# Kernel tuning notes

Hardware: AMD Instinct MI355X
Metric: run time of the kernel (lower is better)

## Reference

```python
import jax, jax.numpy as jnp
import numpy as np

T, B, I, H, R = 24, 64, 128, 256, 64
CLIP_VAL = 1.0
LN_EPS = 1e-5


def _ln(x, g, b):
    mu = jnp.mean(x, axis=-1, keepdims=True)
    var = jnp.mean(jnp.square(x - mu), axis=-1, keepdims=True)
    return (x - mu) / jnp.sqrt(var + LN_EPS) * g + b


def setup_inputs() -> dict:
    key = jax.random.key(0)
    ks = jax.random.split(key, 12)
    x = jax.random.normal(ks[0], (T, B, I), dtype=jnp.float32)
    h0 = 0.1 * jax.random.normal(ks[1], (B, H), dtype=jnp.float32)
    v0 = 0.1 * jax.random.normal(ks[2], (B, H), dtype=jnp.float32)
    dU0 = 0.01 * jax.random.normal(ks[3], (B, H, H), dtype=jnp.float32)
    trace_e0 = 0.1 * jax.random.normal(ks[4], (B, H), dtype=jnp.float32)
    trace_E0 = 0.01 * jax.random.normal(ks[5], (B, H, H), dtype=jnp.float32)
    # parameters, initialized like the torch module
    x2h_w = jax.random.normal(ks[6], (H + R, I), dtype=jnp.float32) / np.sqrt(I)
    x2h_b = jnp.zeros((H + R,), dtype=jnp.float32)
    h2h_w = jax.random.normal(ks[7], (H + R, H), dtype=jnp.float32) / np.sqrt(H)
    h2h_b = jnp.zeros((H + R,), dtype=jnp.float32)
    lnx_g = jnp.ones((H + R,), dtype=jnp.float32)
    lnx_b = jnp.zeros((H + R,), dtype=jnp.float32)
    lnh_g = jnp.ones((H + R,), dtype=jnp.float32)
    lnh_b = jnp.zeros((H + R,), dtype=jnp.float32)
    alpha = 0.01 * jnp.ones((1, H, H), dtype=jnp.float32)
    mod2h = jnp.ones((1, H, R), dtype=jnp.float32) / R
    tau_v = -jnp.log(1.0 + 5.0 * jax.random.uniform(ks[8], (1, H), dtype=jnp.float32))
    tau_U = -2.0 * jnp.ones((1, H, H), dtype=jnp.float32)
    tau_E = -1.0 * jnp.ones((1, H, H), dtype=jnp.float32)
    return dict(x=x, h0=h0, v0=v0, dU0=dU0, trace_e0=trace_e0, trace_E0=trace_E0,
                x2h_w=x2h_w, x2h_b=x2h_b, h2h_w=h2h_w, h2h_b=h2h_b,
                lnx_g=lnx_g, lnx_b=lnx_b, lnh_g=lnh_g, lnh_b=lnh_b,
                alpha=alpha, mod2h=mod2h, tau_v=tau_v, tau_U=tau_U, tau_E=tau_E)


def reference(x, h0, v0, dU0, trace_e0, trace_E0,
              x2h_w, x2h_b, h2h_w, h2h_b,
              lnx_g, lnx_b, lnh_g, lnh_b,
              alpha, mod2h, tau_v, tau_U, tau_E):
    ra = jax.nn.relu(alpha)                      # [1,H,H]
    sv = jax.nn.sigmoid(tau_v)                   # [1,H]
    sU = jax.nn.sigmoid(tau_U)                   # [1,H,H]
    sE = jax.nn.sigmoid(tau_E)                   # [1,H,H]
    W_hh = h2h_w[:H, :]                          # [H,H]
    denom = ra + 1e-8
    dU_hi = jax.nn.relu(CLIP_VAL - W_hh) / denom  # [1,H,H]
    dU_lo = -jax.nn.relu(CLIP_VAL + W_hh) / denom

    def step(carry, x_t):
        v, h, dU, te, tE = carry
        Wx = _ln(x_t @ x2h_w.T + x2h_b, lnx_g, lnx_b)   # [B,H+R]
        Wh = _ln(h @ h2h_w.T + h2h_b, lnh_g, lnh_b)     # [B,H+R]
        dv = Wx[:, :H] + Wh[:, :H] + jnp.einsum('bij,bj->bi', ra * dU, h)
        v = (1.0 - sv) * v + sv * dv
        nh = jax.nn.relu(v)                              # activation='relu'
        mod = jnp.einsum('hr,br->bh', mod2h[0], jax.nn.relu(Wx[:, H:] + Wh[:, H:]))
        nte = (1.0 - sv) * te + sv * h
        ntE = (1.0 - sE) * tE + sE * (nh[:, :, None] * te[:, None, :]
                                      - nte[:, :, None] * h[:, None, :])
        dU = (1.0 - sU) * dU + sU * mod[:, :, None] * ntE
        dU = jnp.maximum(jnp.minimum(dU, dU_hi), dU_lo)
        return (v, nh, dU, nte, ntE), nh

    (v, h, dU, te, tE), out = jax.lax.scan(step, (v0, h0, dU0, trace_e0, trace_E0), x)
    return (v, h, dU, te, tE, out)
```

## Files before the change

### kernel.cpp

```cpp
#include <hip/hip_runtime.h>

#define T_STEPS 24
#define BB 64
#define I_DIM 128
#define HH 256
#define RR 64
#define HR 320

__global__ __launch_bounds__(256) void k_init_const(
    const float* __restrict__ alpha, const float* __restrict__ tau_U,
    const float* __restrict__ tau_E, const float* __restrict__ tau_v,
    const float* __restrict__ h2h_w,
    float* __restrict__ ra, float* __restrict__ sU, float* __restrict__ sE,
    float* __restrict__ hi, float* __restrict__ lo, float* __restrict__ sv)
{
    int idx = blockIdx.x * 256 + threadIdx.x;
    if (idx >= HH * HH) return;
    float a = alpha[idx]; a = a > 0.f ? a : 0.f;
    ra[idx] = a;
    sU[idx] = 1.f / (1.f + expf(-tau_U[idx]));
    sE[idx] = 1.f / (1.f + expf(-tau_E[idx]));
    float wv = h2h_w[idx];
    float inv = 1.f / (a + 1e-8f);
    float hi_ = 1.0f - wv; hi_ = hi_ > 0.f ? hi_ : 0.f;
    float lo_ = 1.0f + wv; lo_ = lo_ > 0.f ? lo_ : 0.f;
    hi[idx] = hi_ * inv;
    lo[idx] = -lo_ * inv;
    if (idx < HH) sv[idx] = 1.f / (1.f + expf(-tau_v[idx]));
}

__global__ __launch_bounds__(HR) void k_wx(
    const float* __restrict__ x,
    const float* __restrict__ w,
    const float* __restrict__ bias,
    const float* __restrict__ g, const float* __restrict__ be,
    float* __restrict__ Wx)
{
    __shared__ float xs[I_DIM];
    __shared__ float rs[5], rs2[5];
    int row = blockIdx.x;
    int p = threadIdx.x;
    if (p < I_DIM) xs[p] = x[(size_t)row * I_DIM + p];
    __syncthreads();
    const float* wr = w + (size_t)p * I_DIM;
    float acc = bias[p];
    #pragma unroll 8
    for (int k = 0; k < I_DIM; k += 4)
        acc += wr[k]*xs[k] + wr[k+1]*xs[k+1] + wr[k+2]*xs[k+2] + wr[k+3]*xs[k+3];
    float s = acc, s2 = acc * acc;
    int lane = p & 63, wv = p >> 6;
    for (int off = 32; off > 0; off >>= 1) { s += __shfl_down(s, off); s2 += __shfl_down(s2, off); }
    if (lane == 0) { rs[wv] = s; rs2[wv] = s2; }
    __syncthreads();
    float sum = 0.f, sum2 = 0.f;
    #pragma unroll
    for (int q = 0; q < 5; q++) { sum += rs[q]; sum2 += rs2[q]; }
    float mu = sum * (1.f / HR);
    float rstd = rsqrtf(sum2 * (1.f / HR) - mu * mu + 1e-5f);
    Wx[(size_t)row * HR + p] = (acc - mu) * rstd * g[p] + be[p];
}

__global__ __launch_bounds__(256) void k_s0(
    const float* __restrict__ dU0, const float* __restrict__ h0,
    const float* __restrict__ ra, float* __restrict__ s_out)
{
    int r = blockIdx.x * 4 + (threadIdx.x >> 6);
    int lane = threadIdx.x & 63;
    int b = r >> 8, i = r & 255;
    float4 du = ((const float4*)dU0)[(size_t)r * 64 + lane];
    float4 rv = ((const float4*)ra)[(size_t)i * 64 + lane];
    float4 hv = ((const float4*)h0)[(size_t)b * 64 + lane];
    float acc = rv.x*du.x*hv.x + rv.y*du.y*hv.y + rv.z*du.z*hv.z + rv.w*du.w*hv.w;
    for (int off = 32; off > 0; off >>= 1) acc += __shfl_down(acc, off);
    if (lane == 0) s_out[r] = acc;
}

__global__ __launch_bounds__(HR) void k_step_a(
    const float* __restrict__ h_old,
    const float* __restrict__ v_old,
    const float* __restrict__ te_old,
    const float* __restrict__ Wx_t,
    const float* __restrict__ s_in,
    const float* __restrict__ h2h_w,
    const float* __restrict__ h2h_b,
    const float* __restrict__ lnh_g, const float* __restrict__ lnh_b,
    const float* __restrict__ sv,
    const float* __restrict__ mod2h,
    float* __restrict__ v_out,
    float* __restrict__ nh_out,
    float* __restrict__ nte_out,
    float* __restrict__ mod_out)
{
    __shared__ float hs[HH];
    __shared__ float modin[RR];
    __shared__ float rs[5], rs2[5];
    int b = blockIdx.x;
    int p = threadIdx.x;
    if (p < HH) hs[p] = h_old[(size_t)b * HH + p];
    __syncthreads();
    const float* wr = h2h_w + (size_t)p * HH;
    float acc = h2h_b[p];
    #pragma unroll 8
    for (int k = 0; k < HH; k += 4)
        acc += wr[k]*hs[k] + wr[k+1]*hs[k+1] + wr[k+2]*hs[k+2] + wr[k+3]*hs[k+3];
    float s = acc, s2 = acc * acc;
    int lane = p & 63, wv = p >> 6;
    for (int off = 32; off > 0; off >>= 1) { s += __shfl_down(s, off); s2 += __shfl_down(s2, off); }
    if (lane == 0) { rs[wv] = s; rs2[wv] = s2; }
    __syncthreads();
    float sum = 0.f, sum2 = 0.f;
    #pragma unroll
    for (int q = 0; q < 5; q++) { sum += rs[q]; sum2 += rs2[q]; }
    float mu = sum * (1.f / HR);
    float rstd = rsqrtf(sum2 * (1.f / HR) - mu * mu + 1e-5f);
    float wh = (acc - mu) * rstd * lnh_g[p] + lnh_b[p];
    float wx = Wx_t[(size_t)b * HR + p];
    if (p >= HH) {
        float m = wx + wh;
        modin[p - HH] = m > 0.f ? m : 0.f;
    } else {
        float dv = wx + wh + s_in[(size_t)b * HH + p];
        float svp = sv[p];
        float v = (1.f - svp) * v_old[(size_t)b * HH + p] + svp * dv;
        v_out[(size_t)b * HH + p] = v;
        float nh = v > 0.f ? v : 0.f;
        nh_out[(size_t)b * HH + p] = nh;
        nte_out[(size_t)b * HH + p] = (1.f - svp) * te_old[(size_t)b * HH + p] + svp * hs[p];
    }
    __syncthreads();
    if (p < HH) {
        const float* m2 = mod2h + (size_t)p * RR;
        float mm = 0.f;
        #pragma unroll 8
        for (int r = 0; r < RR; r += 4)
            mm += m2[r]*modin[r] + m2[r+1]*modin[r+1] + m2[r+2]*modin[r+2] + m2[r+3]*modin[r+3];
        mod_out[(size_t)b * HH + p] = mm;
    }
}

__global__ __launch_bounds__(256) void k_step_b(
    const float* __restrict__ dU_old, float* __restrict__ dU_new,
    const float* __restrict__ tE_old, float* __restrict__ tE_new,
    const float* __restrict__ nh,
    const float* __restrict__ h_old,
    const float* __restrict__ te_old,
    const float* __restrict__ nte,
    const float* __restrict__ mod,
    const float* __restrict__ ra, const float* __restrict__ sU,
    const float* __restrict__ sE, const float* __restrict__ hi,
    const float* __restrict__ lo,
    float* __restrict__ s_out)
{
    int r = blockIdx.x * 4 + (threadIdx.x >> 6);
    int lane = threadIdx.x & 63;
    int b = r >> 8, i = r & 255;
    size_t rowv = (size_t)r * 64 + lane;
    size_t cv   = (size_t)i * 64 + lane;
    size_t bv   = (size_t)b * 64 + lane;
    float4 du  = ((const float4*)dU_old)[rowv];
    float4 tE  = ((const float4*)tE_old)[rowv];
    float4 raV = ((const float4*)ra)[cv];
    float4 sUV = ((const float4*)sU)[cv];
    float4 sEV = ((const float4*)sE)[cv];
    float4 hiV = ((const float4*)hi)[cv];
    float4 loV = ((const float4*)lo)[cv];
    float4 teV = ((const float4*)te_old)[bv];
    float4 hV  = ((const float4*)h_old)[bv];
    float4 nhJ = ((const float4*)nh)[bv];
    float nhi  = nh[(size_t)b * HH + i];
    float ntei = nte[(size_t)b * HH + i];
    float modi = mod[(size_t)b * HH + i];

    float4 ntE, ndu;
    float acc = 0.f;
#define COMPONENT(c)                                                        \
    {                                                                       \
        float e = (1.f - sEV.c) * tE.c + sEV.c * (nhi * teV.c - ntei * hV.c); \
        float d = (1.f - sUV.c) * du.c + sUV.c * modi * e;                  \
        d = fminf(d, hiV.c); d = fmaxf(d, loV.c);                           \
        ntE.c = e; ndu.c = d;                                               \
        acc += raV.c * d * nhJ.c;                                           \
    }
    COMPONENT(x) COMPONENT(y) COMPONENT(z) COMPONENT(w)
#undef COMPONENT
    ((float4*)tE_new)[rowv] = ntE;
    ((float4*)dU_new)[rowv] = ndu;
    for (int off = 32; off > 0; off >>= 1) acc += __shfl_down(acc, off);
    if (lane == 0) s_out[r] = acc;
}

extern "C" void kernel_launch(void* const* d_in, const int* in_sizes, int n_in,
                              void* d_out, int out_size, void* d_ws, size_t ws_size,
                              hipStream_t stream)
{
    const float* x     = (const float*)d_in[0];
    const float* h0    = (const float*)d_in[1];
    const float* v0    = (const float*)d_in[2];
    const float* dU0   = (const float*)d_in[3];
    const float* te0   = (const float*)d_in[4];
    const float* tE0   = (const float*)d_in[5];
    const float* x2h_w = (const float*)d_in[6];
    const float* x2h_b = (const float*)d_in[7];
    const float* h2h_w = (const float*)d_in[8];
    const float* h2h_b = (const float*)d_in[9];
    const float* lnx_g = (const float*)d_in[10];
    const float* lnx_b = (const float*)d_in[11];
    const float* lnh_g = (const float*)d_in[12];
    const float* lnh_b = (const float*)d_in[13];
    const float* alpha = (const float*)d_in[14];
    const float* mod2h = (const float*)d_in[15];
    const float* tau_v = (const float*)d_in[16];
    const float* tau_U = (const float*)d_in[17];
    const float* tau_E = (const float*)d_in[18];

    float* out  = (float*)d_out;
    float* o_v  = out;
    float* o_h  = out + 16384;
    float* o_dU = out + 32768;
    float* o_te = out + 4227072;
    float* o_tE = out + 4243456;
    float* o_out= out + 8437760;

    float* w = (float*)d_ws;
    float* Wx  = w;  w += (size_t)T_STEPS * BB * HR;
    float* ra  = w;  w += HH * HH;
    float* sU  = w;  w += HH * HH;
    float* sE  = w;  w += HH * HH;
    float* hi  = w;  w += HH * HH;
    float* lo  = w;  w += HH * HH;
    float* sv  = w;  w += 256;
    float* s_buf = w; w += BB * HH;
    float* modb  = w; w += BB * HH;
    float* nteb0 = w; w += BB * HH;
    float* nteb1 = w; w += BB * HH;
    float* nteb[2] = { nteb0, nteb1 };

    k_init_const<<<256, 256, 0, stream>>>(alpha, tau_U, tau_E, tau_v, h2h_w,
                                          ra, sU, sE, hi, lo, sv);
    k_wx<<<T_STEPS * BB, HR, 0, stream>>>(x, x2h_w, x2h_b, lnx_g, lnx_b, Wx);
    k_s0<<<4096, 256, 0, stream>>>(dU0, h0, ra, s_buf);

    for (int t = 0; t < T_STEPS; t++) {
        const float* h_old  = (t == 0) ? h0  : o_out + (size_t)(t - 1) * BB * HH;
        const float* v_old  = (t == 0) ? v0  : o_v;
        const float* te_oldp= (t == 0) ? te0 : nteb[(t + 1) & 1];
        const float* dUo    = (t == 0) ? dU0 : o_dU;
        const float* tEo    = (t == 0) ? tE0 : o_tE;
        float* nh = o_out + (size_t)t * BB * HH;
        k_step_a<<<BB, HR, 0, stream>>>(h_old, v_old, te_oldp,
                                        Wx + (size_t)t * BB * HR, s_buf,
                                        h2h_w, h2h_b, lnh_g, lnh_b, sv, mod2h,
                                        o_v, nh, nteb[t & 1], modb);
        k_step_b<<<4096, 256, 0, stream>>>(dUo, o_dU, tEo, o_tE, nh, h_old,
                                           te_oldp, nteb[t & 1], modb,
                                           ra, sU, sE, hi, lo, s_buf);
    }
    hipMemcpyAsync(o_h,  o_out + (size_t)(T_STEPS - 1) * BB * HH, (size_t)BB * HH * 4,
                   hipMemcpyDeviceToDevice, stream);
    hipMemcpyAsync(o_te, nteb[(T_STEPS - 1) & 1], (size_t)BB * HH * 4,
                   hipMemcpyDeviceToDevice, stream);
}
```

Before: 799.3 us.

## Fuse recurrent scan into one persistent cooperative kernel with register-resident state

Replaces the 48 per-timestep kernel launches with a single cooperative persistent kernel of 512 blocks (8 per batch row). Each block keeps its slice of dU and trace_E in registers for all 24 steps, so the two large B×H×H tensors are read once and written once instead of every step. The h2h matvec for the next step is split across blocks, and steps are separated by grid-wide syncs. This adds grid.sync latency per step and heavy register pressure, and keeps the old multi-launch path as a fallback if the cooperative launch fails.

```diff
diff --git a/kernel.cpp b/kernel.cpp
--- a/kernel.cpp
+++ b/kernel.cpp
@@ -1,4 +1,7 @@
 #include <hip/hip_runtime.h>
+#include <hip/hip_cooperative_groups.h>
+
+namespace cg = cooperative_groups;
 
 #define T_STEPS 24
 #define BB 64
@@ -30,8 +33,7 @@
 }
 
 __global__ __launch_bounds__(HR) void k_wx(
-    const float* __restrict__ x,
-    const float* __restrict__ w,
+    const float* __restrict__ x, const float* __restrict__ w,
     const float* __restrict__ bias,
     const float* __restrict__ g, const float* __restrict__ be,
     float* __restrict__ Wx)
@@ -75,21 +77,208 @@
     if (lane == 0) s_out[r] = acc;
 }
 
+__global__ __launch_bounds__(HR) void k_wh0(
+    const float* __restrict__ h0, const float* __restrict__ w,
+    const float* __restrict__ bias, float* __restrict__ whp)
+{
+    __shared__ float hs[HH];
+    int b = blockIdx.x, p = threadIdx.x;
+    if (p < HH) hs[p] = h0[(size_t)b * HH + p];
+    __syncthreads();
+    const float* wr = w + (size_t)p * HH;
+    float acc = bias[p];
+    #pragma unroll 8
+    for (int k = 0; k < HH; k += 4)
+        acc += wr[k]*hs[k] + wr[k+1]*hs[k+1] + wr[k+2]*hs[k+2] + wr[k+3]*hs[k+3];
+    whp[(size_t)b * HR + p] = acc;
+}
+
+__global__ __launch_bounds__(256, 2) void k_scan(
+    const float* __restrict__ dU0, const float* __restrict__ tE0,
+    const float* __restrict__ h0, const float* __restrict__ v0,
+    const float* __restrict__ te0,
+    const float* __restrict__ Wx,
+    const float* __restrict__ h2h_w, const float* __restrict__ h2h_b,
+    const float* __restrict__ lnh_g, const float* __restrict__ lnh_b,
+    const float* __restrict__ sv_g,
+    const float* __restrict__ mod2h,
+    const float* __restrict__ ra, const float* __restrict__ sU,
+    const float* __restrict__ sE, const float* __restrict__ hi,
+    const float* __restrict__ lo,
+    float* __restrict__ whpA, float* __restrict__ whpB,
+    float* __restrict__ sbufA, float* __restrict__ sbufB,
+    float* __restrict__ o_v, float* __restrict__ o_h, float* __restrict__ o_dU,
+    float* __restrict__ o_te, float* __restrict__ o_tE, float* __restrict__ o_out)
+{
+    cg::grid_group grid = cg::this_grid();
+
+    __shared__ __align__(16) float sh_h[2][HH];
+    __shared__ __align__(16) float sh_te[2][HH];
+    __shared__ float sh_v[HH];
+    __shared__ __align__(16) float sh_modin[RR];
+    __shared__ float sh_red[4], sh_red2[4];
+
+    const int bk  = blockIdx.x;
+    const int b   = bk >> 3;
+    const int g   = bk & 7;
+    const int tid = threadIdx.x;
+    const int row_local = tid >> 4;
+    const int jg  = tid & 15;
+    const int i0  = g * 32 + row_local;
+    const int wv  = tid >> 6;
+    const int lane = tid & 63;
+
+    const float svp = sv_g[tid];
+    const float g0 = lnh_g[tid],  be0 = lnh_b[tid];
+    float g1 = 0.f, be1 = 0.f;
+    if (tid < 64) { g1 = lnh_g[HH + tid]; be1 = lnh_b[HH + tid]; }
+
+    const size_t rbase = ((size_t)(b * HH + i0)) * 64 + jg;
+    const float4* dU0v = (const float4*)dU0;
+    const float4* tE0v = (const float4*)tE0;
+    float4 du[2][4], tEr[2][4];
+    #pragma unroll
+    for (int r = 0; r < 2; ++r) {
+        const size_t rb = rbase + (size_t)r * (16 * 64);
+        #pragma unroll
+        for (int k = 0; k < 4; ++k) {
+            du[r][k]  = dU0v[rb + k * 16];
+            tEr[r][k] = tE0v[rb + k * 16];
+        }
+    }
+
+    const float4* raV4 = (const float4*)ra;
+    const float4* sUV4 = (const float4*)sU;
+    const float4* sEV4 = (const float4*)sE;
+    const float4* hiV4 = (const float4*)hi;
+    const float4* loV4 = (const float4*)lo;
+
+    sh_h[0][tid]  = h0[(size_t)b * HH + tid];
+    sh_te[0][tid] = te0[(size_t)b * HH + tid];
+    sh_v[tid]     = v0[(size_t)b * HH + tid];
+    __syncthreads();
+
+    #pragma unroll 1
+    for (int t = 0; t < T_STEPS; t++) {
+        const int cur = t & 1, nxt = cur ^ 1;
+        const float* whp  = (cur == 0) ? whpA  : whpB;
+        float*       whpn = (cur == 0) ? whpB  : whpA;
+        const float* sbi  = (cur == 0) ? sbufA : sbufB;
+        float*       sbo  = (cur == 0) ? sbufB : sbufA;
+
+        const float* whb = whp + (size_t)b * HR;
+        float p0 = whb[tid];
+        float p1 = (tid < 64) ? whb[HH + tid] : 0.f;
+        float s = p0 + p1, s2 = p0 * p0 + p1 * p1;
+        #pragma unroll
+        for (int off = 32; off > 0; off >>= 1) { s += __shfl_down(s, off); s2 += __shfl_down(s2, off); }
+        if (lane == 0) { sh_red[wv] = s; sh_red2[wv] = s2; }
+        __syncthreads();
+        float sum = sh_red[0] + sh_red[1] + sh_red[2] + sh_red[3];
+        float sum2 = sh_red2[0] + sh_red2[1] + sh_red2[2] + sh_red2[3];
+        float mu = sum * (1.f / HR);
+        float rstd = rsqrtf(sum2 * (1.f / HR) - mu * mu + 1e-5f);
+
+        const float* wx_t = Wx + ((size_t)t * BB + b) * HR;
+        float wh0 = (p0 - mu) * rstd * g0 + be0;
+        float dv = wx_t[tid] + wh0 + sbi[(size_t)b * HH + tid];
+        float vnew = (1.f - svp) * sh_v[tid] + svp * dv;
+        sh_v[tid] = vnew;
+        float nh = vnew > 0.f ? vnew : 0.f;
+        sh_h[nxt][tid] = nh;
+        sh_te[nxt][tid] = (1.f - svp) * sh_te[cur][tid] + svp * sh_h[cur][tid];
+        if (tid < 64) {
+            float wh1 = (p1 - mu) * rstd * g1 + be1;
+            float m = wx_t[HH + tid] + wh1;
+            sh_modin[tid] = m > 0.f ? m : 0.f;
+        }
+        if (g == 0) o_out[((size_t)t * BB + b) * HH + tid] = nh;
+        __syncthreads();
+
+#define COMPONENT(c, jj) { \
+        float teO = sh_te[cur][jj]; float hO = sh_h[cur][jj]; float nhJ = sh_h[nxt][jj]; \
+        float e = (1.f - sEV.c) * TE.c + sEV.c * (nhi * teO - ntei * hO); \
+        float d = (1.f - sUV.c) * DU.c + sUV.c * modi * e; \
+        d = fminf(d, hiV.c); d = fmaxf(d, loV.c); \
+        TE.c = e; DU.c = d; acc += raV.c * d * nhJ; }
+
+        #pragma unroll
+        for (int r = 0; r < 2; ++r) {
+            const int i = i0 + r * 16;
+            float4 m4 = *(const float4*)(mod2h + (size_t)i * RR + jg * 4);
+            float4 mi = *(const float4*)&sh_modin[jg * 4];
+            float macc = m4.x*mi.x + m4.y*mi.y + m4.z*mi.z + m4.w*mi.w;
+            macc += __shfl_down(macc, 8, 16);
+            macc += __shfl_down(macc, 4, 16);
+            macc += __shfl_down(macc, 2, 16);
+            macc += __shfl_down(macc, 1, 16);
+            const float modi = __shfl(macc, 0, 16);
+            const float nhi  = sh_h[nxt][i];
+            const float ntei = sh_te[nxt][i];
+            float acc = 0.f;
+            #pragma unroll
+            for (int k = 0; k < 4; ++k) {
+                const size_t ci = (size_t)i * 64 + jg + k * 16;
+                const float4 raV = raV4[ci]; const float4 sUV = sUV4[ci];
+                const float4 sEV = sEV4[ci]; const float4 hiV = hiV4[ci];
+                const float4 loV = loV4[ci];
+                float4 &DU = du[r][k];
+                float4 &TE = tEr[r][k];
+                const int j0 = k * 64 + jg * 4;
+                COMPONENT(x, j0 + 0) COMPONENT(y, j0 + 1)
+                COMPONENT(z, j0 + 2) COMPONENT(w, j0 + 3)
+            }
+            acc += __shfl_down(acc, 8, 16);
+            acc += __shfl_down(acc, 4, 16);
+            acc += __shfl_down(acc, 2, 16);
+            acc += __shfl_down(acc, 1, 16);
+            if (jg == 0) sbo[(size_t)b * HH + i] = acc;
+        }
+#undef COMPONENT
+
+        if (t != T_STEPS - 1) {
+            #pragma unroll
+            for (int k = 0; k < 10; k++) {
+                int p = g * 40 + wv + 4 * k;
+                float4 wrow = ((const float4*)(h2h_w + (size_t)p * HH))[lane];
+                float4 hv = *(const float4*)&sh_h[nxt][lane * 4];
+                float d = wrow.x*hv.x + wrow.y*hv.y + wrow.z*hv.z + wrow.w*hv.w;
+                #pragma unroll
+                for (int off = 32; off > 0; off >>= 1) d += __shfl_down(d, off);
+                if (lane == 0) whpn[(size_t)b * HR + p] = d + h2h_b[p];
+            }
+            __threadfence();
+            grid.sync();
+        }
+    }
+
+    if (g == 0) {
+        o_v[(size_t)b * HH + tid]  = sh_v[tid];
+        o_h[(size_t)b * HH + tid]  = sh_h[0][tid];
+        o_te[(size_t)b * HH + tid] = sh_te[0][tid];
+    }
+    float4* o_dUv = (float4*)o_dU;
+    float4* o_tEv = (float4*)o_tE;
+    #pragma unroll
+    for (int r = 0; r < 2; ++r) {
+        const size_t rb = rbase + (size_t)r * (16 * 64);
+        #pragma unroll
+        for (int k = 0; k < 4; ++k) {
+            o_dUv[rb + k * 16] = du[r][k];
+            o_tEv[rb + k * 16] = tEr[r][k];
+        }
+    }
+}
+
 __global__ __launch_bounds__(HR) void k_step_a(
-    const float* __restrict__ h_old,
-    const float* __restrict__ v_old,
-    const float* __restrict__ te_old,
-    const float* __restrict__ Wx_t,
+    const float* __restrict__ h_old, const float* __restrict__ v_old,
+    const float* __restrict__ te_old, const float* __restrict__ Wx_t,
     const float* __restrict__ s_in,
-    const float* __restrict__ h2h_w,
-    const float* __restrict__ h2h_b,
+    const float* __restrict__ h2h_w, const float* __restrict__ h2h_b,
     const float* __restrict__ lnh_g, const float* __restrict__ lnh_b,
-    const float* __restrict__ sv,
-    const float* __restrict__ mod2h,
-    float* __restrict__ v_out,
-    float* __restrict__ nh_out,
-    float* __restrict__ nte_out,
-    float* __restrict__ mod_out)
+    const float* __restrict__ sv, const float* __restrict__ mod2h,
+    float* __restrict__ v_out, float* __restrict__ nh_out,
+    float* __restrict__ nte_out, float* __restrict__ mod_out)
 {
     __shared__ float hs[HH];
     __shared__ float modin[RR];
@@ -141,10 +330,8 @@
 __global__ __launch_bounds__(256) void k_step_b(
     const float* __restrict__ dU_old, float* __restrict__ dU_new,
     const float* __restrict__ tE_old, float* __restrict__ tE_new,
-    const float* __restrict__ nh,
-    const float* __restrict__ h_old,
-    const float* __restrict__ te_old,
-    const float* __restrict__ nte,
+    const float* __restrict__ nh, const float* __restrict__ h_old,
+    const float* __restrict__ te_old, const float* __restrict__ nte,
     const float* __restrict__ mod,
     const float* __restrict__ ra, const float* __restrict__ sU,
     const float* __restrict__ sE, const float* __restrict__ hi,
@@ -222,41 +409,58 @@
     float* o_out= out + 8437760;
 
     float* w = (float*)d_ws;
-    float* Wx  = w;  w += (size_t)T_STEPS * BB * HR;
-    float* ra  = w;  w += HH * HH;
-    float* sU  = w;  w += HH * HH;
-    float* sE  = w;  w += HH * HH;
-    float* hi  = w;  w += HH * HH;
-    float* lo  = w;  w += HH * HH;
-    float* sv  = w;  w += 256;
-    float* s_buf = w; w += BB * HH;
-    float* modb  = w; w += BB * HH;
-    float* nteb0 = w; w += BB * HH;
-    float* nteb1 = w; w += BB * HH;
+    float* Wx    = w;  w += (size_t)T_STEPS * BB * HR;
+    float* ra    = w;  w += HH * HH;
+    float* sU    = w;  w += HH * HH;
+    float* sE    = w;  w += HH * HH;
+    float* hi    = w;  w += HH * HH;
+    float* lo    = w;  w += HH * HH;
+    float* sv    = w;  w += 256;
+    float* sbufA = w;  w += BB * HH;
+    float* sbufB = w;  w += BB * HH;
+    float* whpA  = w;  w += BB * HR;
+    float* whpB  = w;  w += BB * HR;
+    float* modb  = w;  w += BB * HH;
+    float* nteb0 = w;  w += BB * HH;
+    float* nteb1 = w;  w += BB * HH;
     float* nteb[2] = { nteb0, nteb1 };
 
     k_init_const<<<256, 256, 0, stream>>>(alpha, tau_U, tau_E, tau_v, h2h_w,
                                           ra, sU, sE, hi, lo, sv);
     k_wx<<<T_STEPS * BB, HR, 0, stream>>>(x, x2h_w, x2h_b, lnx_g, lnx_b, Wx);
-    k_s0<<<4096, 256, 0, stream>>>(dU0, h0, ra, s_buf);
-
-    for (int t = 0; t < T_STEPS; t++) {
-        const float* h_old  = (t == 0) ? h0  : o_out + (size_t)(t - 1) * BB * HH;
-        const float* v_old  = (t == 0) ? v0  : o_v;
-        const float* te_oldp= (t == 0) ? te0 : nteb[(t + 1) & 1];
-        const float* dUo    = (t == 0) ? dU0 : o_dU;
-        const float* tEo    = (t == 0) ? tE0 : o_tE;
-        float* nh = o_out + (size_t)t * BB * HH;
-        k_step_a<<<BB, HR, 0, stream>>>(h_old, v_old, te_oldp,
-                                        Wx + (size_t)t * BB * HR, s_buf,
-                                        h2h_w, h2h_b, lnh_g, lnh_b, sv, mod2h,
-                                        o_v, nh, nteb[t & 1], modb);
-        k_step_b<<<4096, 256, 0, stream>>>(dUo, o_dU, tEo, o_tE, nh, h_old,
-                                           te_oldp, nteb[t & 1], modb,
-                                           ra, sU, sE, hi, lo, s_buf);
-    }
-    hipMemcpyAsync(o_h,  o_out + (size_t)(T_STEPS - 1) * BB * HH, (size_t)BB * HH * 4,
-                   hipMemcpyDeviceToDevice, stream);
-    hipMemcpyAsync(o_te, nteb[(T_STEPS - 1) & 1], (size_t)BB * HH * 4,
-                   hipMemcpyDeviceToDevice, stream);
-}
+    k_s0<<<4096, 256, 0, stream>>>(dU0, h0, ra, sbufA);
+    k_wh0<<<BB, HR, 0, stream>>>(h0, h2h_w, h2h_b, whpA);
+
+    void* args[] = {
+        (void*)&dU0, (void*)&tE0, (void*)&h0, (void*)&v0, (void*)&te0,
+        (void*)&Wx, (void*)&h2h_w, (void*)&h2h_b, (void*)&lnh_g, (void*)&lnh_b,
+        (void*)&sv, (void*)&mod2h,
+        (void*)&ra, (void*)&sU, (void*)&sE, (void*)&hi, (void*)&lo,
+        (void*)&whpA, (void*)&whpB, (void*)&sbufA, (void*)&sbufB,
+        (void*)&o_v, (void*)&o_h, (void*)&o_dU, (void*)&o_te, (void*)&o_tE,
+        (void*)&o_out
+    };
+    hipError_t cerr = hipLaunchCooperativeKernel((void*)k_scan, dim3(512),
+                                                 dim3(256), args, 0, stream);
+    if (cerr != hipSuccess) {
+        for (int t = 0; t < T_STEPS; t++) {
+            const float* h_old  = (t == 0) ? h0  : o_out + (size_t)(t - 1) * BB * HH;
+            const float* v_old  = (t == 0) ? v0  : o_v;
+            const float* te_oldp= (t == 0) ? te0 : nteb[(t + 1) & 1];
+            const float* dUo    = (t == 0) ? dU0 : o_dU;
+            const float* tEo    = (t == 0) ? tE0 : o_tE;
+            float* nh = o_out + (size_t)t * BB * HH;
+            k_step_a<<<BB, HR, 0, stream>>>(h_old, v_old, te_oldp,
+                                            Wx + (size_t)t * BB * HR, sbufA,
+                                            h2h_w, h2h_b, lnh_g, lnh_b, sv, mod2h,
+                                            o_v, nh, nteb[t & 1], modb);
+            k_step_b<<<4096, 256, 0, stream>>>(dUo, o_dU, tEo, o_tE, nh, h_old,
+                                               te_oldp, nteb[t & 1], modb,
+                                               ra, sU, sE, hi, lo, sbufA);
+        }
+        hipMemcpyAsync(o_h,  o_out + (size_t)(T_STEPS - 1) * BB * HH,
+                       (size_t)BB * HH * 4, hipMemcpyDeviceToDevice, stream);
+        hipMemcpyAsync(o_te, nteb[(T_STEPS - 1) & 1], (size_t)BB * HH * 4,
+                       hipMemcpyDeviceToDevice, stream);
+    }
+}
```

Measured after the change: 2.649 ms. 3.31x slower.

## Fuse all timesteps into one persistent per-batch kernel with register/LDS-resident state

Applied to the files above, without the earlier changes.

Replaces the 48 per-step launches with a single kernel of 64 blocks (one per batch row) of 1024 threads that loops over all timesteps. The dU state is held in registers, and the tE state is split between registers and LDS, so the per-step HBM round trips of the 256x256 state are removed. Constant tensors are rearranged into a swizzled layout so that coalesced float4 loads match the new thread mapping. The trade-off is that only 64 blocks run, leaving most CUs idle, and register pressure is high, which may cause spills.

```diff
diff --git a/kernel.cpp b/kernel.cpp
--- a/kernel.cpp
+++ b/kernel.cpp
@@ -6,6 +6,8 @@
 #define HH 256
 #define RR 64
 #define HR 320
+#define NREG_TE 7
+#define NLDS_TE 9
 
 __global__ __launch_bounds__(256) void k_init_const(
     const float* __restrict__ alpha, const float* __restrict__ tau_U,
@@ -16,22 +18,24 @@
 {
     int idx = blockIdx.x * 256 + threadIdx.x;
     if (idx >= HH * HH) return;
+    int i = idx >> 8, j = idx & 255;
+    int c = j >> 4, qq = (j >> 2) & 3, e = j & 3;
+    int sidx = (c * 1024 + i * 4 + qq) * 4 + e;
     float a = alpha[idx]; a = a > 0.f ? a : 0.f;
-    ra[idx] = a;
-    sU[idx] = 1.f / (1.f + expf(-tau_U[idx]));
-    sE[idx] = 1.f / (1.f + expf(-tau_E[idx]));
+    ra[sidx] = a;
+    sU[sidx] = 1.f / (1.f + expf(-tau_U[idx]));
+    sE[sidx] = 1.f / (1.f + expf(-tau_E[idx]));
     float wv = h2h_w[idx];
     float inv = 1.f / (a + 1e-8f);
     float hi_ = 1.0f - wv; hi_ = hi_ > 0.f ? hi_ : 0.f;
     float lo_ = 1.0f + wv; lo_ = lo_ > 0.f ? lo_ : 0.f;
-    hi[idx] = hi_ * inv;
-    lo[idx] = -lo_ * inv;
+    hi[sidx] = hi_ * inv;
+    lo[sidx] = -lo_ * inv;
     if (idx < HH) sv[idx] = 1.f / (1.f + expf(-tau_v[idx]));
 }
 
 __global__ __launch_bounds__(HR) void k_wx(
-    const float* __restrict__ x,
-    const float* __restrict__ w,
+    const float* __restrict__ x, const float* __restrict__ w,
     const float* __restrict__ bias,
     const float* __restrict__ g, const float* __restrict__ be,
     float* __restrict__ Wx)
@@ -60,133 +64,212 @@
     Wx[(size_t)row * HR + p] = (acc - mu) * rstd * g[p] + be[p];
 }
 
-__global__ __launch_bounds__(256) void k_s0(
-    const float* __restrict__ dU0, const float* __restrict__ h0,
-    const float* __restrict__ ra, float* __restrict__ s_out)
+__global__ __launch_bounds__(1024) void k_batch(
+    const float* __restrict__ dU0, const float* __restrict__ tE0,
+    const float* __restrict__ h0, const float* __restrict__ v0,
+    const float* __restrict__ te0,
+    const float* __restrict__ Wx,
+    const float* __restrict__ h2h_w, const float* __restrict__ h2h_b,
+    const float* __restrict__ lnh_g, const float* __restrict__ lnh_b,
+    const float* __restrict__ sv_g,
+    const float* __restrict__ mod2h,
+    const float* __restrict__ raS, const float* __restrict__ sUS,
+    const float* __restrict__ sES, const float* __restrict__ hiS,
+    const float* __restrict__ loS,
+    float* __restrict__ o_v, float* __restrict__ o_h, float* __restrict__ o_dU,
+    float* __restrict__ o_te, float* __restrict__ o_tE, float* __restrict__ o_out)
 {
-    int r = blockIdx.x * 4 + (threadIdx.x >> 6);
-    int lane = threadIdx.x & 63;
-    int b = r >> 8, i = r & 255;
-    float4 du = ((const float4*)dU0)[(size_t)r * 64 + lane];
-    float4 rv = ((const float4*)ra)[(size_t)i * 64 + lane];
-    float4 hv = ((const float4*)h0)[(size_t)b * 64 + lane];
-    float acc = rv.x*du.x*hv.x + rv.y*du.y*hv.y + rv.z*du.z*hv.z + rv.w*du.w*hv.w;
-    for (int off = 32; off > 0; off >>= 1) acc += __shfl_down(acc, off);
-    if (lane == 0) s_out[r] = acc;
-}
-
-__global__ __launch_bounds__(HR) void k_step_a(
-    const float* __restrict__ h_old,
-    const float* __restrict__ v_old,
-    const float* __restrict__ te_old,
-    const float* __restrict__ Wx_t,
-    const float* __restrict__ s_in,
-    const float* __restrict__ h2h_w,
-    const float* __restrict__ h2h_b,
-    const float* __restrict__ lnh_g, const float* __restrict__ lnh_b,
-    const float* __restrict__ sv,
-    const float* __restrict__ mod2h,
-    float* __restrict__ v_out,
-    float* __restrict__ nh_out,
-    float* __restrict__ nte_out,
-    float* __restrict__ mod_out)
-{
-    __shared__ float hs[HH];
-    __shared__ float modin[RR];
-    __shared__ float rs[5], rs2[5];
-    int b = blockIdx.x;
-    int p = threadIdx.x;
-    if (p < HH) hs[p] = h_old[(size_t)b * HH + p];
-    __syncthreads();
-    const float* wr = h2h_w + (size_t)p * HH;
-    float acc = h2h_b[p];
-    #pragma unroll 8
-    for (int k = 0; k < HH; k += 4)
-        acc += wr[k]*hs[k] + wr[k+1]*hs[k+1] + wr[k+2]*hs[k+2] + wr[k+3]*hs[k+3];
-    float s = acc, s2 = acc * acc;
-    int lane = p & 63, wv = p >> 6;
-    for (int off = 32; off > 0; off >>= 1) { s += __shfl_down(s, off); s2 += __shfl_down(s2, off); }
-    if (lane == 0) { rs[wv] = s; rs2[wv] = s2; }
-    __syncthreads();
-    float sum = 0.f, sum2 = 0.f;
-    #pragma unroll
-    for (int q = 0; q < 5; q++) { sum += rs[q]; sum2 += rs2[q]; }
-    float mu = sum * (1.f / HR);
-    float rstd = rsqrtf(sum2 * (1.f / HR) - mu * mu + 1e-5f);
-    float wh = (acc - mu) * rstd * lnh_g[p] + lnh_b[p];
-    float wx = Wx_t[(size_t)b * HR + p];
-    if (p >= HH) {
-        float m = wx + wh;
-        modin[p - HH] = m > 0.f ? m : 0.f;
-    } else {
-        float dv = wx + wh + s_in[(size_t)b * HH + p];
-        float svp = sv[p];
-        float v = (1.f - svp) * v_old[(size_t)b * HH + p] + svp * dv;
-        v_out[(size_t)b * HH + p] = v;
-        float nh = v > 0.f ? v : 0.f;
-        nh_out[(size_t)b * HH + p] = nh;
-        nte_out[(size_t)b * HH + p] = (1.f - svp) * te_old[(size_t)b * HH + p] + svp * hs[p];
-    }
-    __syncthreads();
-    if (p < HH) {
-        const float* m2 = mod2h + (size_t)p * RR;
-        float mm = 0.f;
-        #pragma unroll 8
-        for (int r = 0; r < RR; r += 4)
-            mm += m2[r]*modin[r] + m2[r+1]*modin[r+1] + m2[r+2]*modin[r+2] + m2[r+3]*modin[r+3];
-        mod_out[(size_t)b * HH + p] = mm;
-    }
-}
-
-__global__ __launch_bounds__(256) void k_step_b(
-    const float* __restrict__ dU_old, float* __restrict__ dU_new,
-    const float* __restrict__ tE_old, float* __restrict__ tE_new,
-    const float* __restrict__ nh,
-    const float* __restrict__ h_old,
-    const float* __restrict__ te_old,
-    const float* __restrict__ nte,
-    const float* __restrict__ mod,
-    const float* __restrict__ ra, const float* __restrict__ sU,
-    const float* __restrict__ sE, const float* __restrict__ hi,
-    const float* __restrict__ lo,
-    float* __restrict__ s_out)
-{
-    int r = blockIdx.x * 4 + (threadIdx.x >> 6);
-    int lane = threadIdx.x & 63;
-    int b = r >> 8, i = r & 255;
-    size_t rowv = (size_t)r * 64 + lane;
-    size_t cv   = (size_t)i * 64 + lane;
-    size_t bv   = (size_t)b * 64 + lane;
-    float4 du  = ((const float4*)dU_old)[rowv];
-    float4 tE  = ((const float4*)tE_old)[rowv];
-    float4 raV = ((const float4*)ra)[cv];
-    float4 sUV = ((const float4*)sU)[cv];
-    float4 sEV = ((const float4*)sE)[cv];
-    float4 hiV = ((const float4*)hi)[cv];
-    float4 loV = ((const float4*)lo)[cv];
-    float4 teV = ((const float4*)te_old)[bv];
-    float4 hV  = ((const float4*)h_old)[bv];
-    float4 nhJ = ((const float4*)nh)[bv];
-    float nhi  = nh[(size_t)b * HH + i];
-    float ntei = nte[(size_t)b * HH + i];
-    float modi = mod[(size_t)b * HH + i];
-
-    float4 ntE, ndu;
-    float acc = 0.f;
-#define COMPONENT(c)                                                        \
-    {                                                                       \
-        float e = (1.f - sEV.c) * tE.c + sEV.c * (nhi * teV.c - ntei * hV.c); \
-        float d = (1.f - sUV.c) * du.c + sUV.c * modi * e;                  \
-        d = fminf(d, hiV.c); d = fmaxf(d, loV.c);                           \
-        ntE.c = e; ndu.c = d;                                               \
-        acc += raV.c * d * nhJ.c;                                           \
-    }
-    COMPONENT(x) COMPONENT(y) COMPONENT(z) COMPONENT(w)
-#undef COMPONENT
-    ((float4*)tE_new)[rowv] = ntE;
-    ((float4*)dU_new)[rowv] = ndu;
-    for (int off = 32; off > 0; off >>= 1) acc += __shfl_down(acc, off);
-    if (lane == 0) s_out[r] = acc;
+    __shared__ __align__(16) float4 tE_lds[NLDS_TE * 1024];
+    __shared__ __align__(16) float sh_h[2][HH];
+    __shared__ __align__(16) float sh_te[2][HH];
+    __shared__ float sh_v[HH];
+    __shared__ float sh_s[HH];
+    __shared__ __align__(16) float sh_modin[RR];
+    __shared__ float sh_red[5], sh_red2[5];
+
+    const int b   = blockIdx.x;
+    const int t0  = threadIdx.x;
+    const int i   = t0 >> 2;
+    const int qq  = t0 & 3;
+    const int wv  = t0 >> 6;
+    const int lane = t0 & 63;
+
+    float g0 = 0.f, be0 = 0.f, hb = 0.f, svp = 0.f;
+    const float4* wr4 = (const float4*)h2h_w;
+    if (t0 < HR) {
+        g0 = lnh_g[t0]; be0 = lnh_b[t0]; hb = h2h_b[t0];
+        wr4 = (const float4*)(h2h_w + (size_t)t0 * HH);
+        if (t0 < HH) svp = sv_g[t0];
+    }
+
+    const float4* raS4 = (const float4*)raS;
+    const float4* sUS4 = (const float4*)sUS;
+    const float4* sES4 = (const float4*)sES;
+    const float4* hiS4 = (const float4*)hiS;
+    const float4* loS4 = (const float4*)loS;
+    const float4* m2h4 = (const float4*)mod2h;
+
+    const size_t sbase = ((size_t)b * HH + i) * 64 + qq;
+    const float4* dU0v = (const float4*)dU0;
+    const float4* tE0v = (const float4*)tE0;
+    float4 duR[16];
+    float4 teR[NREG_TE];
+    #pragma unroll
+    for (int c = 0; c < 16; ++c) duR[c] = dU0v[sbase + c * 4];
+    #pragma unroll
+    for (int c = 0; c < NREG_TE; ++c) teR[c] = tE0v[sbase + c * 4];
+    #pragma unroll
+    for (int c2 = 0; c2 < NLDS_TE; ++c2)
+        tE_lds[c2 * 1024 + t0] = tE0v[sbase + (NREG_TE + c2) * 4];
+
+    if (t0 < HH) {
+        sh_h[0][t0]  = h0[(size_t)b * HH + t0];
+        sh_te[0][t0] = te0[(size_t)b * HH + t0];
+        sh_v[t0]     = v0[(size_t)b * HH + t0];
+    }
+    __syncthreads();
+
+    {
+        float acc = 0.f;
+        #pragma unroll
+        for (int c = 0; c < 16; ++c) {
+            const float4 raV = raS4[c * 1024 + t0];
+            const int j0 = c * 16 + qq * 4;
+            const float4 h4 = *(const float4*)&sh_h[0][j0];
+            const float4 d = duR[c];
+            acc += raV.x*d.x*h4.x + raV.y*d.y*h4.y + raV.z*d.z*h4.z + raV.w*d.w*h4.w;
+        }
+        acc += __shfl_xor(acc, 1, 4);
+        acc += __shfl_xor(acc, 2, 4);
+        if (qq == 0) sh_s[i] = acc;
+    }
+    __syncthreads();
+
+    #pragma unroll 1
+    for (int t = 0; t < T_STEPS; ++t) {
+        const int cur = t & 1, nxt = cur ^ 1;
+
+        float pre = 0.f;
+        if (t0 < HR) {
+            float a0 = hb, a1 = 0.f;
+            #pragma unroll 8
+            for (int k = 0; k < 64; k += 2) {
+                float4 w0 = wr4[k],     w1 = wr4[k+1];
+                float4 h0v = *(const float4*)&sh_h[cur][k << 2];
+                float4 h1v = *(const float4*)&sh_h[cur][(k+1) << 2];
+                a0 += w0.x*h0v.x + w0.y*h0v.y + w0.z*h0v.z + w0.w*h0v.w;
+                a1 += w1.x*h1v.x + w1.y*h1v.y + w1.z*h1v.z + w1.w*h1v.w;
+            }
+            pre = a0 + a1;
+            float s = pre, s2 = pre * pre;
+            #pragma unroll
+            for (int off = 32; off > 0; off >>= 1) {
+                s += __shfl_down(s, off); s2 += __shfl_down(s2, off);
+            }
+            if (lane == 0) { sh_red[wv] = s; sh_red2[wv] = s2; }
+        }
+        __syncthreads();
+
+        {
+            float sum = 0.f, sum2 = 0.f;
+            #pragma unroll
+            for (int q = 0; q < 5; ++q) { sum += sh_red[q]; sum2 += sh_red2[q]; }
+            float mu = sum * (1.f / HR);
+            float rstd = rsqrtf(sum2 * (1.f / HR) - mu * mu + 1e-5f);
+            if (t0 < HR) {
+                float wh = (pre - mu) * rstd * g0 + be0;
+                float wx = Wx[((size_t)t * BB + b) * HR + t0];
+                if (t0 < HH) {
+                    float dv = wx + wh + sh_s[t0];
+                    float vnew = (1.f - svp) * sh_v[t0] + svp * dv;
+                    sh_v[t0] = vnew;
+                    float nh = vnew > 0.f ? vnew : 0.f;
+                    sh_h[nxt][t0] = nh;
+                    sh_te[nxt][t0] = (1.f - svp) * sh_te[cur][t0] + svp * sh_h[cur][t0];
+                    o_out[((size_t)t * BB + b) * HH + t0] = nh;
+                } else {
+                    float m = wx + wh;
+                    sh_modin[t0 - HH] = m > 0.f ? m : 0.f;
+                }
+            }
+        }
+        __syncthreads();
+
+        {
+            float macc = 0.f;
+            #pragma unroll
+            for (int e = 0; e < 4; ++e) {
+                const float4 m4 = m2h4[i * 16 + qq * 4 + e];
+                const float4 mi = *(const float4*)&sh_modin[qq * 16 + e * 4];
+                macc += m4.x*mi.x + m4.y*mi.y + m4.z*mi.z + m4.w*mi.w;
+            }
+            macc += __shfl_xor(macc, 1, 4);
+            macc += __shfl_xor(macc, 2, 4);
+            const float modi = macc;
+            const float nhi  = sh_h[nxt][i];
+            const float ntei = sh_te[nxt][i];
+            float acc = 0.f;
+
+#define UPDC(cc, TE) { \
+            const float4 raV = raS4[(cc) * 1024 + t0]; \
+            const float4 sUV = sUS4[(cc) * 1024 + t0]; \
+            const float4 sEV = sES4[(cc) * 1024 + t0]; \
+            const float4 hiV = hiS4[(cc) * 1024 + t0]; \
+            const float4 loV = loS4[(cc) * 1024 + t0]; \
+            const int j0 = (cc) * 16 + qq * 4; \
+            const float4 teo = *(const float4*)&sh_te[cur][j0]; \
+            const float4 ho  = *(const float4*)&sh_h[cur][j0]; \
+            const float4 hn  = *(const float4*)&sh_h[nxt][j0]; \
+            float4 DU = duR[cc]; \
+            { float ev = (1.f-sEV.x)*TE.x + sEV.x*(nhi*teo.x - ntei*ho.x); \
+              float dd = (1.f-sUV.x)*DU.x + sUV.x*modi*ev; \
+              dd = fminf(dd, hiV.x); dd = fmaxf(dd, loV.x); \
+              TE.x = ev; DU.x = dd; acc += raV.x*dd*hn.x; } \
+            { float ev = (1.f-sEV.y)*TE.y + sEV.y*(nhi*teo.y - ntei*ho.y); \
+              float dd = (1.f-sUV.y)*DU.y + sUV.y*modi*ev; \
+              dd = fminf(dd, hiV.y); dd = fmaxf(dd, loV.y); \
+              TE.y = ev; DU.y = dd; acc += raV.y*dd*hn.y; } \
+            { float ev = (1.f-sEV.z)*TE.z + sEV.z*(nhi*teo.z - ntei*ho.z); \
+              float dd = (1.f-sUV.z)*DU.z + sUV.z*modi*ev; \
+              dd = fminf(dd, hiV.z); dd = fmaxf(dd, loV.z); \
+              TE.z = ev; DU.z = dd; acc += raV.z*dd*hn.z; } \
+            { float ev = (1.f-sEV.w)*TE.w + sEV.w*(nhi*teo.w - ntei*ho.w); \
+              float dd = (1.f-sUV.w)*DU.w + sUV.w*modi*ev; \
+              dd = fminf(dd, hiV.w); dd = fmaxf(dd, loV.w); \
+              TE.w = ev; DU.w = dd; acc += raV.w*dd*hn.w; } \
+            duR[cc] = DU; }
+
+            #pragma unroll
+            for (int c = 0; c < NREG_TE; ++c) { UPDC(c, teR[c]); }
+            #pragma unroll
+            for (int c2 = 0; c2 < NLDS_TE; ++c2) {
+                float4 TE = tE_lds[c2 * 1024 + t0];
+                UPDC(NREG_TE + c2, TE);
+                tE_lds[c2 * 1024 + t0] = TE;
+            }
+#undef UPDC
+
+            acc += __shfl_xor(acc, 1, 4);
+            acc += __shfl_xor(acc, 2, 4);
+            if (qq == 0) sh_s[i] = acc;
+        }
+    }
+
+    __syncthreads();
+    if (t0 < HH) {
+        o_v[(size_t)b * HH + t0]  = sh_v[t0];
+        o_h[(size_t)b * HH + t0]  = sh_h[0][t0];
+        o_te[(size_t)b * HH + t0] = sh_te[0][t0];
+    }
+    float4* o_dUv = (float4*)o_dU;
+    float4* o_tEv = (float4*)o_tE;
+    #pragma unroll
+    for (int c = 0; c < 16; ++c) o_dUv[sbase + c * 4] = duR[c];
+    #pragma unroll
+    for (int c = 0; c < NREG_TE; ++c) o_tEv[sbase + c * 4] = teR[c];
+    #pragma unroll
+    for (int c2 = 0; c2 < NLDS_TE; ++c2)
+        o_tEv[sbase + (NREG_TE + c2) * 4] = tE_lds[c2 * 1024 + t0];
 }
 
 extern "C" void kernel_launch(void* const* d_in, const int* in_sizes, int n_in,
@@ -229,34 +312,12 @@
     float* hi  = w;  w += HH * HH;
     float* lo  = w;  w += HH * HH;
     float* sv  = w;  w += 256;
-    float* s_buf = w; w += BB * HH;
-    float* modb  = w; w += BB * HH;
-    float* nteb0 = w; w += BB * HH;
-    float* nteb1 = w; w += BB * HH;
-    float* nteb[2] = { nteb0, nteb1 };
 
     k_init_const<<<256, 256, 0, stream>>>(alpha, tau_U, tau_E, tau_v, h2h_w,
                                           ra, sU, sE, hi, lo, sv);
     k_wx<<<T_STEPS * BB, HR, 0, stream>>>(x, x2h_w, x2h_b, lnx_g, lnx_b, Wx);
-    k_s0<<<4096, 256, 0, stream>>>(dU0, h0, ra, s_buf);
-
-    for (int t = 0; t < T_STEPS; t++) {
-        const float* h_old  = (t == 0) ? h0  : o_out + (size_t)(t - 1) * BB * HH;
-        const float* v_old  = (t == 0) ? v0  : o_v;
-        const float* te_oldp= (t == 0) ? te0 : nteb[(t + 1) & 1];
-        const float* dUo    = (t == 0) ? dU0 : o_dU;
-        const float* tEo    = (t == 0) ? tE0 : o_tE;
-        float* nh = o_out + (size_t)t * BB * HH;
-        k_step_a<<<BB, HR, 0, stream>>>(h_old, v_old, te_oldp,
-                                        Wx + (size_t)t * BB * HR, s_buf,
-                                        h2h_w, h2h_b, lnh_g, lnh_b, sv, mod2h,
-                                        o_v, nh, nteb[t & 1], modb);
-        k_step_b<<<4096, 256, 0, stream>>>(dUo, o_dU, tEo, o_tE, nh, h_old,
-                                           te_oldp, nteb[t & 1], modb,
-                                           ra, sU, sE, hi, lo, s_buf);
-    }
-    hipMemcpyAsync(o_h,  o_out + (size_t)(T_STEPS - 1) * BB * HH, (size_t)BB * HH * 4,
-                   hipMemcpyDeviceToDevice, stream);
-    hipMemcpyAsync(o_te, nteb[(T_STEPS - 1) & 1], (size_t)BB * HH * 4,
-                   hipMemcpyDeviceToDevice, stream);
+    k_batch<<<BB, 1024, 0, stream>>>(dU0, tE0, h0, v0, te0, Wx,
+                                     h2h_w, h2h_b, lnh_g, lnh_b, sv, mod2h,
+                                     ra, sU, sE, hi, lo,
+                                     o_v, o_h, o_dU, o_te, o_tE, o_out);
 }
```

Result: slower. 1.542 ms (+92.9%).
